# Performance work log

Hardware: AMD Instinct MI355X
Metric: run time of the kernel (lower is better)

The kernel has to match this reference:

```python
import jax, jax.numpy as jnp
import numpy as np

NUM_CODEBOOKS = 2
CODEBOOK_SIZE = 256
OUT_GROUP = 1
IN_GROUP = 8
IN_FEATURES = 4096
OUT_FEATURES = 11008


def setup_inputs() -> dict:
    key = jax.random.key(0)
    k1, k2, k3, k4, k5 = jax.random.split(key, 5)
    num_out_groups = OUT_FEATURES // OUT_GROUP
    num_in_groups = IN_FEATURES // IN_GROUP
    x = jax.random.normal(k1, (4, 2048, IN_FEATURES), dtype=jnp.float32)
    codes = jax.random.randint(k2, (num_out_groups, num_in_groups, NUM_CODEBOOKS), 0, CODEBOOK_SIZE, dtype=jnp.int32)
    codebooks = jax.random.normal(k3, (NUM_CODEBOOKS, CODEBOOK_SIZE, OUT_GROUP, IN_GROUP), dtype=jnp.float32) * 0.05
    scales = jax.random.uniform(k4, (num_out_groups, 1, 1, 1), dtype=jnp.float32)
    bias = jax.random.normal(k5, (OUT_FEATURES,), dtype=jnp.float32)
    return {"x": x, "codes": codes, "codebooks": codebooks, "scales": scales, "bias": bias}


def _dequantize_weight(codes, codebooks, scales):
    # codes: [Og, Ig, C] int; codebooks: [C, K, og, ig]; scales: [Og,1,1,1]
    C = codebooks.shape[0]
    og, ig = codebooks.shape[2], codebooks.shape[3]
    Og, Ig = codes.shape[0], codes.shape[1]
    # gather per-codebook vectors: result [Og, Ig, C, og, ig]
    w = codebooks[jnp.arange(C)[None, None, :], codes]
    w = w.sum(axis=2)                      # [Og, Ig, og, ig] (additive quantization)
    w = w * scales                         # broadcast [Og,1,1,1]
    w = w.transpose(0, 2, 1, 3)            # [Og, og, Ig, ig]
    return w.reshape(Og * og, Ig * ig)     # [out_features, in_features]


def reference(x, codes, codebooks, scales, bias):
    W = _dequantize_weight(codes, codebooks, scales)
    return jnp.einsum('bsi,oi->bso', x, W) + bias
```

## Files before the change

### kernel.cpp

```cpp
#include <hip/hip_runtime.h>
#include <hip/hip_bf16.h>
#include <stdint.h>

#define IN_FEATURES 4096
#define OUT_FEATURES 11008
#define M_ROWS 8192
#define NUM_IN_GROUPS 512
#define CB_SIZE 256

typedef _Float16 f16x8 __attribute__((ext_vector_type(8)));
typedef float f32x4 __attribute__((ext_vector_type(4)));

__global__ __launch_bounds__(256) void dequant_w_kernel(
    const int* __restrict__ codes, const float* __restrict__ cbs,
    _Float16* __restrict__ W)
{
  const int idx = blockIdx.x * 256 + threadIdx.x;
  const int2 c = ((const int2*)codes)[idx];
  const float4* e0 = (const float4*)(cbs + (size_t)c.x * 8);
  const float4* e1 = (const float4*)(cbs + (size_t)CB_SIZE * 8 + (size_t)c.y * 8);
  const float4 a0 = e0[0], a1 = e0[1];
  const float4 b0 = e1[0], b1 = e1[1];
  f16x8 w;
  w[0] = (_Float16)(a0.x + b0.x);
  w[1] = (_Float16)(a0.y + b0.y);
  w[2] = (_Float16)(a0.z + b0.z);
  w[3] = (_Float16)(a0.w + b0.w);
  w[4] = (_Float16)(a1.x + b1.x);
  w[5] = (_Float16)(a1.y + b1.y);
  w[6] = (_Float16)(a1.z + b1.z);
  w[7] = (_Float16)(a1.w + b1.w);
  *(f16x8*)(W + (size_t)idx * 8) = w;
}

__global__ __launch_bounds__(256) void convert_x_kernel(
    const float* __restrict__ x, _Float16* __restrict__ X)
{
  const size_t i = ((size_t)blockIdx.x * 256 + threadIdx.x) * 8;
  const float4 a = *(const float4*)(x + i);
  const float4 b = *(const float4*)(x + i + 4);
  f16x8 v;
  v[0] = (_Float16)a.x; v[1] = (_Float16)a.y;
  v[2] = (_Float16)a.z; v[3] = (_Float16)a.w;
  v[4] = (_Float16)b.x; v[5] = (_Float16)b.y;
  v[6] = (_Float16)b.z; v[7] = (_Float16)b.w;
  *(f16x8*)(X + i) = v;
}

#define BM 128
#define BN 128
#define BK 64
#define NT_M (M_ROWS / BM)

__global__ __launch_bounds__(256, 2) void gemm_f16_kernel(
    const _Float16* __restrict__ X, const _Float16* __restrict__ W,
    const float* __restrict__ scales, const float* __restrict__ bias,
    float* __restrict__ out)
{
  __shared__ _Float16 lds_a[BM * BK];
  __shared__ _Float16 lds_b[BN * BK];

  const int nt = blockIdx.x / NT_M;
  const int mt = blockIdx.x % NT_M;
  const int m0 = mt * BM, n0 = nt * BN;
  const int lane = threadIdx.x & 63;
  const int wave = threadIdx.x >> 6;
  const int wm = wave >> 1, wn = wave & 1;
  const int r16 = lane & 15;
  const int koff = (lane >> 4) * 8;

  f32x4 acc[4][4] = {};

  for (int kt = 0; kt < IN_FEATURES / BK; ++kt) {
    __syncthreads();
    const size_t kb = (size_t)kt * BK;
    #pragma unroll
    for (int it = 0; it < 4; ++it) {
      const int cbase = (wave * 4 + it) * 64;
      const int c = cbase + lane;
      const int row = c >> 3;
      const int col = (c & 7) * 8;
      __builtin_amdgcn_global_load_lds(
          (const __attribute__((address_space(1))) void*)(X + (size_t)(m0 + row) * IN_FEATURES + kb + col),
          (__attribute__((address_space(3))) void*)(lds_a + (size_t)cbase * 8),
          16, 0, 0);
    }
    #pragma unroll
    for (int it = 0; it < 4; ++it) {
      const int cbase = (wave * 4 + it) * 64;
      const int c = cbase + lane;
      const int row = c >> 3;
      const int col = (c & 7) * 8;
      __builtin_amdgcn_global_load_lds(
          (const __attribute__((address_space(1))) void*)(W + (size_t)(n0 + row) * IN_FEATURES + kb + col),
          (__attribute__((address_space(3))) void*)(lds_b + (size_t)cbase * 8),
          16, 0, 0);
    }
    __syncthreads();

    #pragma unroll
    for (int kk = 0; kk < BK; kk += 32) {
      f16x8 af[4], bf[4];
      #pragma unroll
      for (int m = 0; m < 4; ++m)
        af[m] = *(const f16x8*)(lds_a + (wm * 64 + m * 16 + r16) * BK + kk + koff);
      #pragma unroll
      for (int n = 0; n < 4; ++n)
        bf[n] = *(const f16x8*)(lds_b + (wn * 64 + n * 16 + r16) * BK + kk + koff);
      #pragma unroll
      for (int m = 0; m < 4; ++m) {
        #pragma unroll
        for (int n = 0; n < 4; ++n)
          acc[m][n] = __builtin_amdgcn_mfma_f32_16x16x32_f16(af[m], bf[n], acc[m][n], 0, 0, 0);
      }
    }
  }

  const int crow = (lane >> 4) * 4;
  #pragma unroll
  for (int n = 0; n < 4; ++n) {
    const int col = n0 + wn * 64 + n * 16 + r16;
    const float s = scales[col];
    const float bb = bias[col];
    #pragma unroll
    for (int m = 0; m < 4; ++m) {
      const int rowb = m0 + wm * 64 + m * 16 + crow;
      #pragma unroll
      for (int r = 0; r < 4; ++r)
        out[(size_t)(rowb + r) * OUT_FEATURES + col] = acc[m][n][r] * s + bb;
    }
  }
}

__global__ __launch_bounds__(256) void naive_kernel(
    const float* __restrict__ x, const int* __restrict__ codes,
    const float* __restrict__ cbs, const float* __restrict__ scales,
    const float* __restrict__ bias, float* __restrict__ out)
{
  __shared__ float xrow[IN_FEATURES];
  const int m = blockIdx.x;
  for (int i = threadIdx.x; i < IN_FEATURES; i += 256)
    xrow[i] = x[(size_t)m * IN_FEATURES + i];
  __syncthreads();
  for (int o = threadIdx.x; o < OUT_FEATURES; o += 256) {
    float acc = 0.f;
    const int2* crow = (const int2*)codes + (size_t)o * NUM_IN_GROUPS;
    for (int g = 0; g < NUM_IN_GROUPS; ++g) {
      const int2 c = crow[g];
      const float* e0 = cbs + (size_t)c.x * 8;
      const float* e1 = cbs + (size_t)CB_SIZE * 8 + (size_t)c.y * 8;
      const float* xr = xrow + g * 8;
      #pragma unroll
      for (int j = 0; j < 8; ++j) acc += (e0[j] + e1[j]) * xr[j];
    }
    out[(size_t)m * OUT_FEATURES + o] = acc * scales[o] + bias[o];
  }
}

extern "C" void kernel_launch(void* const* d_in, const int* in_sizes, int n_in,
                              void* d_out, int out_size, void* d_ws, size_t ws_size,
                              hipStream_t stream) {
  const float* x      = (const float*)d_in[0];
  const int*   codes  = (const int*)d_in[1];
  const float* cbs    = (const float*)d_in[2];
  const float* scales = (const float*)d_in[3];
  const float* bias   = (const float*)d_in[4];
  float* out = (float*)d_out;

  const size_t W_BYTES = (size_t)OUT_FEATURES * IN_FEATURES * sizeof(_Float16);
  const size_t X_BYTES = (size_t)M_ROWS * IN_FEATURES * sizeof(_Float16);

  if (ws_size < W_BYTES + X_BYTES) {
    naive_kernel<<<M_ROWS, 256, 0, stream>>>(x, codes, cbs, scales, bias, out);
    return;
  }

  _Float16* W = (_Float16*)d_ws;
  _Float16* X = (_Float16*)((char*)d_ws + W_BYTES);

  dequant_w_kernel<<<(OUT_FEATURES * NUM_IN_GROUPS) / 256, 256, 0, stream>>>(codes, cbs, W);
  convert_x_kernel<<<(M_ROWS * IN_FEATURES / 8) / 256, 256, 0, stream>>>(x, X);
  gemm_f16_kernel<<<(M_ROWS / BM) * (OUT_FEATURES / BN), 256, 0, stream>>>(X, W, scales, bias, out);
}
```

Measured before the change: 882.4 us.

## Rewrite GEMM as 256x256 double-buffered 8-wave kernel with swizzled LDS

Replaces the 128x128 single-buffered f16 MFMA GEMM with a 256x256 tile kernel using 512 threads. It double-buffers the 128KB LDS so the next K-tile's global-to-LDS loads overlap with compute. It also splits each K step into four barrier-separated MFMA phases with s_setprio, XOR-swizzles the LDS layout to avoid bank conflicts, and remaps block IDs across XCDs for cache locality. The larger tiles cut global traffic per FLOP, but they raise register and LDS pressure, which allows only one block per CU.

```diff
diff --git a/kernel.cpp b/kernel.cpp
--- a/kernel.cpp
+++ b/kernel.cpp
@@ -2,11 +2,11 @@
 #include <hip/hip_bf16.h>
 #include <stdint.h>
 
-#define IN_FEATURES 4096
-#define OUT_FEATURES 11008
+#define IN_F 4096
+#define OUT_F 11008
 #define M_ROWS 8192
-#define NUM_IN_GROUPS 512
-#define CB_SIZE 256
+#define NIG 512
+#define CBSZ 256
 
 typedef _Float16 f16x8 __attribute__((ext_vector_type(8)));
 typedef float f32x4 __attribute__((ext_vector_type(4)));
@@ -18,7 +18,7 @@
   const int idx = blockIdx.x * 256 + threadIdx.x;
   const int2 c = ((const int2*)codes)[idx];
   const float4* e0 = (const float4*)(cbs + (size_t)c.x * 8);
-  const float4* e1 = (const float4*)(cbs + (size_t)CB_SIZE * 8 + (size_t)c.y * 8);
+  const float4* e1 = (const float4*)(cbs + (size_t)CBSZ * 8 + (size_t)c.y * 8);
   const float4 a0 = e0[0], a1 = e0[1];
   const float4 b0 = e1[0], b1 = e1[1];
   f16x8 w;
@@ -47,89 +47,151 @@
   *(f16x8*)(X + i) = v;
 }
 
-#define BM 128
-#define BN 128
+#define BM 256
+#define BN 256
 #define BK 64
-#define NT_M (M_ROWS / BM)
-
-__global__ __launch_bounds__(256, 2) void gemm_f16_kernel(
-    const _Float16* __restrict__ X, const _Float16* __restrict__ W,
+#define NKT (IN_F / BK)
+#define GRID_MT (M_ROWS / BM)
+#define GRID_NT (OUT_F / BN)
+
+__global__ __launch_bounds__(512, 2) void gemm_8phase(
+    const _Float16* __restrict__ X, const _Float16* __restrict__ Wd,
     const float* __restrict__ scales, const float* __restrict__ bias,
     float* __restrict__ out)
 {
-  __shared__ _Float16 lds_a[BM * BK];
-  __shared__ _Float16 lds_b[BN * BK];
-
-  const int nt = blockIdx.x / NT_M;
-  const int mt = blockIdx.x % NT_M;
+  __shared__ char smem[131072];
+
+  const int cpx = (GRID_MT * GRID_NT) >> 3;
+  const int wg = (blockIdx.x & 7) * cpx + (blockIdx.x >> 3);
+  const int mt = wg & 31, nt = wg >> 5;
   const int m0 = mt * BM, n0 = nt * BN;
-  const int lane = threadIdx.x & 63;
-  const int wave = threadIdx.x >> 6;
-  const int wm = wave >> 1, wn = wave & 1;
+
+  const int t = threadIdx.x;
+  const int wave = t >> 6, lane = t & 63;
+  const int wm = wave >> 2, wn = wave & 3;
   const int r16 = lane & 15;
-  const int koff = (lane >> 4) * 8;
-
-  f32x4 acc[4][4] = {};
-
-  for (int kt = 0; kt < IN_FEATURES / BK; ++kt) {
+  const int koff2 = (lane >> 4) << 4;
+  const int Xr = ((r16 & 8) << 2) | ((r16 & 4) << 2);
+  const int laneoff = r16 * 64 + (koff2 ^ Xr);
+
+  const int s_row0 = ((t >> 7) << 4) | ((t >> 2) & 15);
+  const int s_col  = (((t >> 6) & 1) << 5) | (((((t & 3) << 4) ^ (t & 48))) >> 1);
+  const _Float16* asrc = X  + (size_t)(m0 + s_row0) * IN_F + s_col;
+  const _Float16* bsrc = Wd + (size_t)(n0 + s_row0) * IN_F + s_col;
+  const int s_dst = wave * 1024;
+
+  f32x4 acc[8][4] = {};
+  f16x8 alo[4][2], ahi[4][2], blo[2][2], bhi[2][2];
+
+#define STAGE(kt, b) do {                                                     \
+    const _Float16* _a = asrc + (size_t)(kt) * BK;                            \
+    const _Float16* _b = bsrc + (size_t)(kt) * BK;                            \
+    _Pragma("unroll")                                                         \
+    for (int i = 0; i < 4; ++i)                                               \
+      __builtin_amdgcn_global_load_lds(                                       \
+        (const __attribute__((address_space(1))) void*)(_a + (size_t)i * 64 * IN_F), \
+        (__attribute__((address_space(3))) void*)(smem + (b) * 65536 + i * 8192 + s_dst), \
+        16, 0, 0);                                                            \
+    _Pragma("unroll")                                                         \
+    for (int i = 0; i < 4; ++i)                                               \
+      __builtin_amdgcn_global_load_lds(                                       \
+        (const __attribute__((address_space(1))) void*)(_b + (size_t)i * 64 * IN_F), \
+        (__attribute__((address_space(3))) void*)(smem + (b) * 65536 + 32768 + i * 8192 + s_dst), \
+        16, 0, 0);                                                            \
+  } while (0)
+
+  STAGE(0, 0);
+  __syncthreads();
+
+  for (int j = 0; j < NKT; ++j) {
+    const int cur = j & 1;
+    const char* Ab = smem + cur * 65536;
+    const char* Bb = smem + cur * 65536 + 32768;
+
+    if (j + 1 < NKT) STAGE(j + 1, cur ^ 1);
+    #pragma unroll
+    for (int m = 0; m < 4; ++m)
+      #pragma unroll
+      for (int k = 0; k < 2; ++k)
+        alo[m][k] = *(const f16x8*)(Ab + (wm * 8 + m) * 2048 + k * 1024 + laneoff);
+    #pragma unroll
+    for (int n = 0; n < 2; ++n)
+      #pragma unroll
+      for (int k = 0; k < 2; ++k)
+        blo[n][k] = *(const f16x8*)(Bb + (wn * 4 + n) * 2048 + k * 1024 + laneoff);
+    __builtin_amdgcn_s_barrier();
+    __builtin_amdgcn_s_setprio(1);
+    #pragma unroll
+    for (int k = 0; k < 2; ++k)
+      #pragma unroll
+      for (int m = 0; m < 4; ++m)
+        #pragma unroll
+        for (int n = 0; n < 2; ++n)
+          acc[m][n] = __builtin_amdgcn_mfma_f32_16x16x32_f16(alo[m][k], blo[n][k], acc[m][n], 0, 0, 0);
+    __builtin_amdgcn_s_setprio(0);
+    __builtin_amdgcn_s_barrier();
+
+    #pragma unroll
+    for (int n = 0; n < 2; ++n)
+      #pragma unroll
+      for (int k = 0; k < 2; ++k)
+        bhi[n][k] = *(const f16x8*)(Bb + (wn * 4 + 2 + n) * 2048 + k * 1024 + laneoff);
+    __builtin_amdgcn_s_barrier();
+    __builtin_amdgcn_s_setprio(1);
+    #pragma unroll
+    for (int k = 0; k < 2; ++k)
+      #pragma unroll
+      for (int m = 0; m < 4; ++m)
+        #pragma unroll
+        for (int n = 0; n < 2; ++n)
+          acc[m][2 + n] = __builtin_amdgcn_mfma_f32_16x16x32_f16(alo[m][k], bhi[n][k], acc[m][2 + n], 0, 0, 0);
+    __builtin_amdgcn_s_setprio(0);
+    __builtin_amdgcn_s_barrier();
+
+    #pragma unroll
+    for (int m = 0; m < 4; ++m)
+      #pragma unroll
+      for (int k = 0; k < 2; ++k)
+        ahi[m][k] = *(const f16x8*)(Ab + (wm * 8 + 4 + m) * 2048 + k * 1024 + laneoff);
+    __builtin_amdgcn_s_barrier();
+    __builtin_amdgcn_s_setprio(1);
+    #pragma unroll
+    for (int k = 0; k < 2; ++k)
+      #pragma unroll
+      for (int m = 0; m < 4; ++m)
+        #pragma unroll
+        for (int n = 0; n < 2; ++n)
+          acc[4 + m][2 + n] = __builtin_amdgcn_mfma_f32_16x16x32_f16(ahi[m][k], bhi[n][k], acc[4 + m][2 + n], 0, 0, 0);
+    __builtin_amdgcn_s_setprio(0);
+    __builtin_amdgcn_s_barrier();
+
+    __builtin_amdgcn_s_setprio(1);
+    #pragma unroll
+    for (int k = 0; k < 2; ++k)
+      #pragma unroll
+      for (int m = 0; m < 4; ++m)
+        #pragma unroll
+        for (int n = 0; n < 2; ++n)
+          acc[4 + m][n] = __builtin_amdgcn_mfma_f32_16x16x32_f16(ahi[m][k], blo[n][k], acc[4 + m][n], 0, 0, 0);
+    __builtin_amdgcn_s_setprio(0);
     __syncthreads();
-    const size_t kb = (size_t)kt * BK;
-    #pragma unroll
-    for (int it = 0; it < 4; ++it) {
-      const int cbase = (wave * 4 + it) * 64;
-      const int c = cbase + lane;
-      const int row = c >> 3;
-      const int col = (c & 7) * 8;
-      __builtin_amdgcn_global_load_lds(
-          (const __attribute__((address_space(1))) void*)(X + (size_t)(m0 + row) * IN_FEATURES + kb + col),
-          (__attribute__((address_space(3))) void*)(lds_a + (size_t)cbase * 8),
-          16, 0, 0);
-    }
-    #pragma unroll
-    for (int it = 0; it < 4; ++it) {
-      const int cbase = (wave * 4 + it) * 64;
-      const int c = cbase + lane;
-      const int row = c >> 3;
-      const int col = (c & 7) * 8;
-      __builtin_amdgcn_global_load_lds(
-          (const __attribute__((address_space(1))) void*)(W + (size_t)(n0 + row) * IN_FEATURES + kb + col),
-          (__attribute__((address_space(3))) void*)(lds_b + (size_t)cbase * 8),
-          16, 0, 0);
-    }
-    __syncthreads();
-
-    #pragma unroll
-    for (int kk = 0; kk < BK; kk += 32) {
-      f16x8 af[4], bf[4];
-      #pragma unroll
-      for (int m = 0; m < 4; ++m)
-        af[m] = *(const f16x8*)(lds_a + (wm * 64 + m * 16 + r16) * BK + kk + koff);
-      #pragma unroll
-      for (int n = 0; n < 4; ++n)
-        bf[n] = *(const f16x8*)(lds_b + (wn * 64 + n * 16 + r16) * BK + kk + koff);
-      #pragma unroll
-      for (int m = 0; m < 4; ++m) {
-        #pragma unroll
-        for (int n = 0; n < 4; ++n)
-          acc[m][n] = __builtin_amdgcn_mfma_f32_16x16x32_f16(af[m], bf[n], acc[m][n], 0, 0, 0);
-      }
-    }
-  }
-
-  const int crow = (lane >> 4) * 4;
+  }
+
+  const int crow = (lane >> 4) << 2;
   #pragma unroll
-  for (int n = 0; n < 4; ++n) {
-    const int col = n0 + wn * 64 + n * 16 + r16;
+  for (int nf = 0; nf < 4; ++nf) {
+    const int col = n0 + wn * 64 + nf * 16 + r16;
     const float s = scales[col];
     const float bb = bias[col];
     #pragma unroll
-    for (int m = 0; m < 4; ++m) {
-      const int rowb = m0 + wm * 64 + m * 16 + crow;
+    for (int mf = 0; mf < 8; ++mf) {
+      const int rb = m0 + wm * 128 + mf * 16 + crow;
       #pragma unroll
       for (int r = 0; r < 4; ++r)
-        out[(size_t)(rowb + r) * OUT_FEATURES + col] = acc[m][n][r] * s + bb;
+        out[(size_t)(rb + r) * OUT_F + col] = acc[mf][nf][r] * s + bb;
     }
   }
+#undef STAGE
 }
 
 __global__ __launch_bounds__(256) void naive_kernel(
@@ -137,23 +199,23 @@
     const float* __restrict__ cbs, const float* __restrict__ scales,
     const float* __restrict__ bias, float* __restrict__ out)
 {
-  __shared__ float xrow[IN_FEATURES];
+  __shared__ float xrow[IN_F];
   const int m = blockIdx.x;
-  for (int i = threadIdx.x; i < IN_FEATURES; i += 256)
-    xrow[i] = x[(size_t)m * IN_FEATURES + i];
+  for (int i = threadIdx.x; i < IN_F; i += 256)
+    xrow[i] = x[(size_t)m * IN_F + i];
   __syncthreads();
-  for (int o = threadIdx.x; o < OUT_FEATURES; o += 256) {
+  for (int o = threadIdx.x; o < OUT_F; o += 256) {
     float acc = 0.f;
-    const int2* crow = (const int2*)codes + (size_t)o * NUM_IN_GROUPS;
-    for (int g = 0; g < NUM_IN_GROUPS; ++g) {
+    const int2* crow = (const int2*)codes + (size_t)o * NIG;
+    for (int g = 0; g < NIG; ++g) {
       const int2 c = crow[g];
       const float* e0 = cbs + (size_t)c.x * 8;
-      const float* e1 = cbs + (size_t)CB_SIZE * 8 + (size_t)c.y * 8;
+      const float* e1 = cbs + (size_t)CBSZ * 8 + (size_t)c.y * 8;
       const float* xr = xrow + g * 8;
       #pragma unroll
       for (int j = 0; j < 8; ++j) acc += (e0[j] + e1[j]) * xr[j];
     }
-    out[(size_t)m * OUT_FEATURES + o] = acc * scales[o] + bias[o];
+    out[(size_t)m * OUT_F + o] = acc * scales[o] + bias[o];
   }
 }
 
@@ -167,8 +229,8 @@
   const float* bias   = (const float*)d_in[4];
   float* out = (float*)d_out;
 
-  const size_t W_BYTES = (size_t)OUT_FEATURES * IN_FEATURES * sizeof(_Float16);
-  const size_t X_BYTES = (size_t)M_ROWS * IN_FEATURES * sizeof(_Float16);
+  const size_t W_BYTES = (size_t)OUT_F * IN_F * sizeof(_Float16);
+  const size_t X_BYTES = (size_t)M_ROWS * IN_F * sizeof(_Float16);
 
   if (ws_size < W_BYTES + X_BYTES) {
     naive_kernel<<<M_ROWS, 256, 0, stream>>>(x, codes, cbs, scales, bias, out);
@@ -178,7 +240,7 @@
   _Float16* W = (_Float16*)d_ws;
   _Float16* X = (_Float16*)((char*)d_ws + W_BYTES);
 
-  dequant_w_kernel<<<(OUT_FEATURES * NUM_IN_GROUPS) / 256, 256, 0, stream>>>(codes, cbs, W);
-  convert_x_kernel<<<(M_ROWS * IN_FEATURES / 8) / 256, 256, 0, stream>>>(x, X);
-  gemm_f16_kernel<<<(M_ROWS / BM) * (OUT_FEATURES / BN), 256, 0, stream>>>(X, W, scales, bias, out);
-}
+  dequant_w_kernel<<<(OUT_F * NIG) / 256, 256, 0, stream>>>(codes, cbs, W);
+  convert_x_kernel<<<(M_ROWS * IN_F / 8) / 256, 256, 0, stream>>>(x, X);
+  gemm_8phase<<<GRID_MT * GRID_NT, 512, 0, stream>>>(X, W, scales, bias, out);
+}
```

New measurement: 925.0 us. 1.05x slower.
